# Performance work log

Measured on AMD Instinct MI355X. Metric: run time of the kernel, lower is better.

## Reference

```python
import jax, jax.numpy as jnp
import numpy as np

B = 4
N_TOTAL = 40000
N_SRC0, N_DST0, E0 = 30000, 15000, 360000
N_DST1, E1 = 7500, 180000
D_IN, OUT = 64, 32
H1, C1 = 8, 8
H2, C2 = 1, OUT
NEG_SLOPE = 0.2


def setup_inputs() -> dict:
    key = jax.random.key(0)
    ks = jax.random.split(key, 16)
    inp = {
        'x': jax.random.normal(ks[0], (B, N_TOTAL, D_IN), dtype=jnp.float32),
        'n_id0': jax.random.randint(ks[1], (N_SRC0,), 0, N_SRC0),
        'res_n_id0': jax.random.randint(ks[2], (N_DST0,), 0, N_SRC0),
        'edge_src0': jax.random.randint(ks[3], (E0,), 0, N_SRC0),
        'edge_dst0': jax.random.randint(ks[4], (E0,), 0, N_DST0),
        'res_n_id1': jax.random.randint(ks[5], (N_DST1,), 0, N_DST0),
        'edge_src1': jax.random.randint(ks[6], (E1,), 0, N_DST0),
        'edge_dst1': jax.random.randint(ks[7], (E1,), 0, N_DST1),
        # GATConv params (Glorot-ish scale)
        'W1': jax.random.normal(ks[8], (D_IN, H1 * C1), dtype=jnp.float32) / np.sqrt(D_IN),
        'att_src1': jax.random.normal(ks[9], (H1, C1), dtype=jnp.float32) / np.sqrt(C1),
        'att_dst1': jax.random.normal(ks[10], (H1, C1), dtype=jnp.float32) / np.sqrt(C1),
        'b1': jnp.zeros((H1 * C1,), dtype=jnp.float32),
        'W2': jax.random.normal(ks[11], (H1 * C1, H2 * C2), dtype=jnp.float32) / np.sqrt(H1 * C1),
        'att_src2': jax.random.normal(ks[12], (H2, C2), dtype=jnp.float32) / np.sqrt(C2),
        'att_dst2': jax.random.normal(ks[13], (H2, C2), dtype=jnp.float32) / np.sqrt(C2),
        'b2': jnp.zeros((H2 * C2,), dtype=jnp.float32),
    }
    return inp


def gat_conv(x_src, x_dst, src, dst, W, a_src, a_dst, bias, n_dst, H, C):
    """Bipartite PyG-style GATConv (concat=True, eval mode, no self-loops)."""
    b = x_src.shape[0]
    hs = (x_src @ W).reshape(b, -1, H, C)            # [B, Ns, H, C]
    hd = (x_dst @ W).reshape(b, -1, H, C)            # [B, Nd, H, C]
    es = jnp.einsum('bnhc,hc->bnh', hs, a_src)       # [B, Ns, H]
    ed = jnp.einsum('bnhc,hc->bnh', hd, a_dst)       # [B, Nd, H]
    e = jax.nn.leaky_relu(es[:, src] + ed[:, dst], NEG_SLOPE)  # [B, E, H]
    eT = jnp.swapaxes(e, 0, 1)                       # [E, B, H] (segment over axis 0)
    m = jax.ops.segment_max(eT, dst, num_segments=n_dst)
    p = jnp.exp(eT - m[dst])
    den = jax.ops.segment_sum(p, dst, num_segments=n_dst)
    alpha = p / den[dst]                             # [E, B, H]
    msg = alpha[..., None] * jnp.swapaxes(hs[:, src], 0, 1)    # [E, B, H, C]
    out = jax.ops.segment_sum(msg, dst, num_segments=n_dst)    # [Nd, B, H, C]
    out = jnp.swapaxes(out, 0, 1).reshape(b, n_dst, H * C)
    return out + bias


def reference(x, n_id0, res_n_id0, edge_src0, edge_dst0, res_n_id1, edge_src1,
              edge_dst1, W1, att_src1, att_dst1, b1, W2, att_src2, att_dst2, b2):
    xt = x[:, n_id0, :]                                        # [B, N_SRC0, D_IN]
    h = gat_conv(xt, xt[:, res_n_id0, :], edge_src0, edge_dst0,
                 W1, att_src1, att_dst1, b1, N_DST0, H1, C1)
    h = jax.nn.elu(h)                                          # dropout = identity (eval)
    out = gat_conv(h, h[:, res_n_id1, :], edge_src1, edge_dst1,
                   W2, att_src2, att_dst2, b2, N_DST1, H2, C2)
    return out                                                 # [B, N_DST1, OUT]
```

## Files before the change

### kernel.cpp

```cpp
#include <hip/hip_runtime.h>

#define NB 4
#define NT 40000
#define NS0 30000
#define ND0 15000
#define NE0 360000
#define ND1 7500
#define NE1 180000
#define NEG 0.2f

#define CAP 64
#define K1B ((NB*NS0)/64)
#define SB  ((NE0 + NE1 + 255)/256)

typedef __attribute__((ext_vector_type(8))) short bf8;
typedef __attribute__((ext_vector_type(4))) float f4;

__device__ __forceinline__ unsigned short f2bf(float f) {
    unsigned u = __float_as_uint(f);
    u += 0x7FFF + ((u >> 16) & 1);
    return (unsigned short)(u >> 16);
}
__device__ __forceinline__ float bf_lo(unsigned u) { return __uint_as_float(u << 16); }
__device__ __forceinline__ float bf_hi(unsigned u) { return __uint_as_float(u & 0xFFFF0000u); }

__global__ __launch_bounds__(256) void kA_gemm_scat(
        const float* __restrict__ x, const int* __restrict__ n_id0,
        const float* __restrict__ W1, const float* __restrict__ a_src,
        const float* __restrict__ a_dst,
        unsigned short* __restrict__ ht1b, float* __restrict__ es1, float* __restrict__ ed1,
        const int* __restrict__ esrc0, const int* __restrict__ edst0,
        const int* __restrict__ esrc1, const int* __restrict__ edst1,
        int* __restrict__ cur0, int* __restrict__ cur1,
        int* __restrict__ srcsort0, int* __restrict__ srcsort1) {
    __shared__ unsigned short xtb[64*72];
    __shared__ unsigned short wtb[64*72];
    __shared__ float asl[64], adl[64];
    if (blockIdx.x >= K1B) {
        int t = (blockIdx.x - K1B) * 256 + threadIdx.x;
        if (t < NE0) {
            int d = edst0[t];
            int pos = atomicAdd(&cur0[d], 1);
            if (pos < CAP) srcsort0[d*CAP + pos] = esrc0[t];
        } else if (t < NE0 + NE1) {
            int e = t - NE0;
            int d = edst1[e];
            int pos = atomicAdd(&cur1[d], 1);
            if (pos < CAP) srcsort1[d*CAP + pos] = esrc1[e];
        }
        return;
    }
    int t = threadIdx.x;
    {
        int k = t >> 2, nb = (t & 3) * 16;
        const float* wrow = &W1[k*64 + nb];
        #pragma unroll
        for (int j = 0; j < 16; j += 4) {
            float4 v = *(const float4*)&wrow[j];
            wtb[(nb+j+0)*72 + k] = f2bf(v.x);
            wtb[(nb+j+1)*72 + k] = f2bf(v.y);
            wtb[(nb+j+2)*72 + k] = f2bf(v.z);
            wtb[(nb+j+3)*72 + k] = f2bf(v.w);
        }
    }
    if (t < 64) { asl[t] = a_src[t]; adl[t] = a_dst[t]; }
    {
        int rr = t & 63;
        int q4 = t >> 6;
        int row_s = blockIdx.x * 64 + rr;
        int bs = row_s / NS0;
        int ns = row_s - bs * NS0;
        const float* xrow = x + ((size_t)(bs * NT + n_id0[ns])) * 64;
        #pragma unroll
        for (int j = 0; j < 4; ++j) {
            int k = q4 * 16 + j * 4;
            float4 v = *(const float4*)&xrow[k];
            ushort4 u;
            u.x = f2bf(v.x); u.y = f2bf(v.y); u.z = f2bf(v.z); u.w = f2bf(v.w);
            *(ushort4*)&xtb[rr*72 + k] = u;
        }
    }
    __syncthreads();
    int w = t >> 6, lane = t & 63, quad = lane >> 4, cl = lane & 15;
    int arow = 16*w + cl;
    bf8 a0 = *(const bf8*)&xtb[arow*72 + quad*8];
    bf8 a1 = *(const bf8*)&xtb[arow*72 + 32 + quad*8];
    f4 acc[4];
    #pragma unroll
    for (int sub = 0; sub < 4; ++sub) {
        int n = sub*16 + cl;
        bf8 b0 = *(const bf8*)&wtb[n*72 + quad*8];
        bf8 b1 = *(const bf8*)&wtb[n*72 + 32 + quad*8];
        f4 c = {0.f, 0.f, 0.f, 0.f};
        c = __builtin_amdgcn_mfma_f32_16x16x32_bf16(a0, b0, c, 0, 0, 0);
        c = __builtin_amdgcn_mfma_f32_16x16x32_bf16(a1, b1, c, 0, 0, 0);
        acc[sub] = c;
    }
    int rbase = blockIdx.x*64 + 16*w + quad*4;
    #pragma unroll
    for (int sub = 0; sub < 4; ++sub)
        #pragma unroll
        for (int r = 0; r < 4; ++r)
            ht1b[(size_t)(rbase + r)*64 + sub*16 + cl] = f2bf(acc[sub][r]);
    #pragma unroll
    for (int r = 0; r < 4; ++r) {
        #pragma unroll
        for (int sub = 0; sub < 4; ++sub) {
            int col = sub*16 + cl;
            float ps = acc[sub][r] * asl[col];
            float pd = acc[sub][r] * adl[col];
            ps += __shfl_xor(ps, 1); ps += __shfl_xor(ps, 2); ps += __shfl_xor(ps, 4);
            pd += __shfl_xor(pd, 1); pd += __shfl_xor(pd, 2); pd += __shfl_xor(pd, 4);
            if ((cl & 7) == 0) {
                int h = sub*2 + (cl >> 3);
                es1[(rbase + r)*8 + h] = ps;
                ed1[(rbase + r)*8 + h] = pd;
            }
        }
    }
}

__global__ __launch_bounds__(256) void k3_agg1(
        const int* __restrict__ srcsort0, const int* __restrict__ cur0,
        const int* __restrict__ res0,
        const float* __restrict__ es1, const float* __restrict__ ed1,
        const unsigned short* __restrict__ ht1b, const float* __restrict__ b1,
        float* __restrict__ agg1) {
    int b = blockIdx.x / (ND0/4);
    int chunk = blockIdx.x - b * (ND0/4);
    int d = chunk * 4 + (threadIdx.x >> 6);
    int lane = threadIdx.x & 63;
    int grp = lane >> 3;
    int c = lane & 7;
    int dn = res0[d];
    float edv = ed1[(b*NS0 + dn)*8 + c];
    int start = d * CAP;
    int cnt = cur0[d];
    const float* esb = es1 + (size_t)b*NS0*8;
    const unsigned short* htb = ht1b + (size_t)b*NS0*64;
    float acc[8] = {};
    float wsum = 0.f;
    int i = grp;
    bool v0 = i      < cnt, v1 = i + 8  < cnt,
         v2 = i + 16 < cnt, v3 = i + 24 < cnt;
    int s0 = v0 ? srcsort0[start + i]      : 0;
    int s1 = v1 ? srcsort0[start + i + 8]  : 0;
    int s2 = v2 ? srcsort0[start + i + 16] : 0;
    int s3 = v3 ? srcsort0[start + i + 24] : 0;
    for (;;) {
        float e0 = esb[s0*8 + c], e1 = esb[s1*8 + c];
        float e2 = esb[s2*8 + c], e3 = esb[s3*8 + c];
        uint4 h0 = *(const uint4*)&htb[(size_t)s0*64 + c*8];
        uint4 h1 = *(const uint4*)&htb[(size_t)s1*64 + c*8];
        uint4 h2 = *(const uint4*)&htb[(size_t)s2*64 + c*8];
        uint4 h3 = *(const uint4*)&htb[(size_t)s3*64 + c*8];
        int ni = i + 32;
        bool nv0 = ni      < cnt, nv1 = ni + 8  < cnt,
             nv2 = ni + 16 < cnt, nv3 = ni + 24 < cnt;
        int t0 = nv0 ? srcsort0[start + ni]      : 0;
        int t1 = nv1 ? srcsort0[start + ni + 8]  : 0;
        int t2 = nv2 ? srcsort0[start + ni + 16] : 0;
        int t3 = nv3 ? srcsort0[start + ni + 24] : 0;
        e0 += edv; e1 += edv; e2 += edv; e3 += edv;
        e0 = e0 > 0.f ? e0 : NEG * e0;
        e1 = e1 > 0.f ? e1 : NEG * e1;
        e2 = e2 > 0.f ? e2 : NEG * e2;
        e3 = e3 > 0.f ? e3 : NEG * e3;
        float w0 = v0 ? __expf(e0) : 0.f;
        float w1 = v1 ? __expf(e1) : 0.f;
        float w2 = v2 ? __expf(e2) : 0.f;
        float w3 = v3 ? __expf(e3) : 0.f;
        acc[0] = fmaf(w0, bf_lo(h0.x), acc[0]); acc[1] = fmaf(w0, bf_hi(h0.x), acc[1]);
        acc[2] = fmaf(w0, bf_lo(h0.y), acc[2]); acc[3] = fmaf(w0, bf_hi(h0.y), acc[3]);
        acc[4] = fmaf(w0, bf_lo(h0.z), acc[4]); acc[5] = fmaf(w0, bf_hi(h0.z), acc[5]);
        acc[6] = fmaf(w0, bf_lo(h0.w), acc[6]); acc[7] = fmaf(w0, bf_hi(h0.w), acc[7]);
        acc[0] = fmaf(w1, bf_lo(h1.x), acc[0]); acc[1] = fmaf(w1, bf_hi(h1.x), acc[1]);
        acc[2] = fmaf(w1, bf_lo(h1.y), acc[2]); acc[3] = fmaf(w1, bf_hi(h1.y), acc[3]);
        acc[4] = fmaf(w1, bf_lo(h1.z), acc[4]); acc[5] = fmaf(w1, bf_hi(h1.z), acc[5]);
        acc[6] = fmaf(w1, bf_lo(h1.w), acc[6]); acc[7] = fmaf(w1, bf_hi(h1.w), acc[7]);
        acc[0] = fmaf(w2, bf_lo(h2.x), acc[0]); acc[1] = fmaf(w2, bf_hi(h2.x), acc[1]);
        acc[2] = fmaf(w2, bf_lo(h2.y), acc[2]); acc[3] = fmaf(w2, bf_hi(h2.y), acc[3]);
        acc[4] = fmaf(w2, bf_lo(h2.z), acc[4]); acc[5] = fmaf(w2, bf_hi(h2.z), acc[5]);
        acc[6] = fmaf(w2, bf_lo(h2.w), acc[6]); acc[7] = fmaf(w2, bf_hi(h2.w), acc[7]);
        acc[0] = fmaf(w3, bf_lo(h3.x), acc[0]); acc[1] = fmaf(w3, bf_hi(h3.x), acc[1]);
        acc[2] = fmaf(w3, bf_lo(h3.y), acc[2]); acc[3] = fmaf(w3, bf_hi(h3.y), acc[3]);
        acc[4] = fmaf(w3, bf_lo(h3.z), acc[4]); acc[5] = fmaf(w3, bf_hi(h3.z), acc[5]);
        acc[6] = fmaf(w3, bf_lo(h3.w), acc[6]); acc[7] = fmaf(w3, bf_hi(h3.w), acc[7]);
        wsum += (w0 + w1) + (w2 + w3);
        i = ni; s0 = t0; s1 = t1; s2 = t2; s3 = t3;
        v0 = nv0; v1 = nv1; v2 = nv2; v3 = nv3;
        if (i >= cnt) break;
    }
    #pragma unroll
    for (int j = 0; j < 8; ++j) {
        acc[j] += __shfl_xor(acc[j], 8);
        acc[j] += __shfl_xor(acc[j], 16);
        acc[j] += __shfl_xor(acc[j], 32);
    }
    wsum += __shfl_xor(wsum, 8); wsum += __shfl_xor(wsum, 16); wsum += __shfl_xor(wsum, 32);
    if (grp == 0) {
        float inv = cnt > 0 ? 1.f / wsum : 0.f;
        float4 b_lo = *(const float4*)&b1[c*8];
        float4 b_hi = *(const float4*)&b1[c*8 + 4];
        float o[8];
        o[0] = acc[0]*inv + b_lo.x; o[1] = acc[1]*inv + b_lo.y;
        o[2] = acc[2]*inv + b_lo.z; o[3] = acc[3]*inv + b_lo.w;
        o[4] = acc[4]*inv + b_hi.x; o[5] = acc[5]*inv + b_hi.y;
        o[6] = acc[6]*inv + b_hi.z; o[7] = acc[7]*inv + b_hi.w;
        #pragma unroll
        for (int j = 0; j < 8; ++j) o[j] = o[j] > 0.f ? o[j] : __expf(o[j]) - 1.f;
        float* orow = &agg1[((size_t)(b*ND0 + d))*64 + c*8];
        *(float4*)&orow[0] = make_float4(o[0], o[1], o[2], o[3]);
        *(float4*)&orow[4] = make_float4(o[4], o[5], o[6], o[7]);
    }
}

__global__ __launch_bounds__(256) void k5_node2(
        const float* __restrict__ h, const float* __restrict__ W2,
        const float* __restrict__ a_src2, const float* __restrict__ a_dst2,
        float* __restrict__ ht2, float* __restrict__ es2, float* __restrict__ ed2) {
    __shared__ float xt[64*132];
    __shared__ float Wl[64*32];
    __shared__ float as2[32], ad2[32];
    int t = threadIdx.x;
    for (int i = t; i < 512; i += 256)
        *(float4*)&Wl[i*4] = *(const float4*)&W2[i*4];
    if (t < 32) { as2[t] = a_src2[t]; ad2[t] = a_dst2[t]; }
    int rr = t & 127;
    int q  = t >> 7;
    int row_s = blockIdx.x * 128 + rr;
    bool valid = row_s < NB*ND0;
    const float* hrow = h + (size_t)row_s * 64;
    #pragma unroll
    for (int j = 0; j < 8; ++j) {
        int k = q * 32 + j * 4;
        float4 v = valid ? *(const float4*)&hrow[k] : make_float4(0.f,0.f,0.f,0.f);
        xt[(k+0)*132 + rr] = v.x;
        xt[(k+1)*132 + rr] = v.y;
        xt[(k+2)*132 + rr] = v.z;
        xt[(k+3)*132 + rr] = v.w;
    }
    __syncthreads();
    int c0 = (t & 7) * 4;
    int r0 = (t >> 3) * 4;
    float acc[4][4] = {};
    #pragma unroll 16
    for (int k = 0; k < 64; ++k) {
        float4 a = *(const float4*)&xt[k*132 + r0];
        float4 w = *(const float4*)&Wl[k*32 + c0];
        acc[0][0] = fmaf(a.x, w.x, acc[0][0]); acc[0][1] = fmaf(a.x, w.y, acc[0][1]);
        acc[0][2] = fmaf(a.x, w.z, acc[0][2]); acc[0][3] = fmaf(a.x, w.w, acc[0][3]);
        acc[1][0] = fmaf(a.y, w.x, acc[1][0]); acc[1][1] = fmaf(a.y, w.y, acc[1][1]);
        acc[1][2] = fmaf(a.y, w.z, acc[1][2]); acc[1][3] = fmaf(a.y, w.w, acc[1][3]);
        acc[2][0] = fmaf(a.z, w.x, acc[2][0]); acc[2][1] = fmaf(a.z, w.y, acc[2][1]);
        acc[2][2] = fmaf(a.z, w.z, acc[2][2]); acc[2][3] = fmaf(a.z, w.w, acc[2][3]);
        acc[3][0] = fmaf(a.w, w.x, acc[3][0]); acc[3][1] = fmaf(a.w, w.y, acc[3][1]);
        acc[3][2] = fmaf(a.w, w.z, acc[3][2]); acc[3][3] = fmaf(a.w, w.w, acc[3][3]);
    }
    float s0 = as2[c0], s1 = as2[c0+1], s2 = as2[c0+2], s3 = as2[c0+3];
    float d0 = ad2[c0], d1 = ad2[c0+1], d2 = ad2[c0+2], d3 = ad2[c0+3];
    #pragma unroll
    for (int i = 0; i < 4; ++i) {
        int row = blockIdx.x * 128 + r0 + i;
        float ps = acc[i][0]*s0 + acc[i][1]*s1 + acc[i][2]*s2 + acc[i][3]*s3;
        float pd = acc[i][0]*d0 + acc[i][1]*d1 + acc[i][2]*d2 + acc[i][3]*d3;
        ps += __shfl_xor(ps, 1); ps += __shfl_xor(ps, 2); ps += __shfl_xor(ps, 4);
        pd += __shfl_xor(pd, 1); pd += __shfl_xor(pd, 2); pd += __shfl_xor(pd, 4);
        if (row < NB*ND0) {
            *(float4*)&ht2[(size_t)row*32 + c0] =
                make_float4(acc[i][0], acc[i][1], acc[i][2], acc[i][3]);
            if ((t & 7) == 0) { es2[row] = ps; ed2[row] = pd; }
        }
    }
}

__global__ __launch_bounds__(256) void k7_agg2(
        const int* __restrict__ srcsort1, const int* __restrict__ cur1,
        const int* __restrict__ res1,
        const float* __restrict__ es2, const float* __restrict__ ed2,
        const float* __restrict__ ht2, const float* __restrict__ b2,
        float* __restrict__ outp) {
    int b = blockIdx.x / (ND1/4);
    int chunk = blockIdx.x - b * (ND1/4);
    int d = chunk * 4 + (threadIdx.x >> 6);
    int lane = threadIdx.x & 63;
    int grp = lane >> 3;
    int c = lane & 7;
    int dn = res1[d];
    float edv = ed2[b*ND0 + dn];
    int start = d * CAP;
    int cnt = cur1[d];
    const float* esb = es2 + (size_t)b*ND0;
    const float* htb = ht2 + (size_t)b*ND0*32;
    float ax = 0.f, ay = 0.f, az = 0.f, aw = 0.f, wsum = 0.f;
    int i = grp;
    bool v0 = i      < cnt, v1 = i + 8  < cnt,
         v2 = i + 16 < cnt, v3 = i + 24 < cnt;
    int s0 = v0 ? srcsort1[start + i]      : 0;
    int s1 = v1 ? srcsort1[start + i + 8]  : 0;
    int s2 = v2 ? srcsort1[start + i + 16] : 0;
    int s3 = v3 ? srcsort1[start + i + 24] : 0;
    for (;;) {
        float lg0 = esb[s0], lg1 = esb[s1], lg2 = esb[s2], lg3 = esb[s3];
        float4 h0 = *(const float4*)&htb[(size_t)s0*32 + c*4];
        float4 h1 = *(const float4*)&htb[(size_t)s1*32 + c*4];
        float4 h2 = *(const float4*)&htb[(size_t)s2*32 + c*4];
        float4 h3 = *(const float4*)&htb[(size_t)s3*32 + c*4];
        int ni = i + 32;
        bool nv0 = ni      < cnt, nv1 = ni + 8  < cnt,
             nv2 = ni + 16 < cnt, nv3 = ni + 24 < cnt;
        int t0 = nv0 ? srcsort1[start + ni]      : 0;
        int t1 = nv1 ? srcsort1[start + ni + 8]  : 0;
        int t2 = nv2 ? srcsort1[start + ni + 16] : 0;
        int t3 = nv3 ? srcsort1[start + ni + 24] : 0;
        lg0 += edv; lg1 += edv; lg2 += edv; lg3 += edv;
        lg0 = lg0 > 0.f ? lg0 : NEG * lg0;
        lg1 = lg1 > 0.f ? lg1 : NEG * lg1;
        lg2 = lg2 > 0.f ? lg2 : NEG * lg2;
        lg3 = lg3 > 0.f ? lg3 : NEG * lg3;
        float w0 = v0 ? __expf(lg0) : 0.f;
        float w1 = v1 ? __expf(lg1) : 0.f;
        float w2 = v2 ? __expf(lg2) : 0.f;
        float w3 = v3 ? __expf(lg3) : 0.f;
        ax = fmaf(w0, h0.x, ax); ay = fmaf(w0, h0.y, ay);
        az = fmaf(w0, h0.z, az); aw = fmaf(w0, h0.w, aw);
        ax = fmaf(w1, h1.x, ax); ay = fmaf(w1, h1.y, ay);
        az = fmaf(w1, h1.z, az); aw = fmaf(w1, h1.w, aw);
        ax = fmaf(w2, h2.x, ax); ay = fmaf(w2, h2.y, ay);
        az = fmaf(w2, h2.z, az); aw = fmaf(w2, h2.w, aw);
        ax = fmaf(w3, h3.x, ax); ay = fmaf(w3, h3.y, ay);
        az = fmaf(w3, h3.z, az); aw = fmaf(w3, h3.w, aw);
        wsum += (w0 + w1) + (w2 + w3);
        i = ni; s0 = t0; s1 = t1; s2 = t2; s3 = t3;
        v0 = nv0; v1 = nv1; v2 = nv2; v3 = nv3;
        if (i >= cnt) break;
    }
    ax += __shfl_xor(ax, 8); ax += __shfl_xor(ax, 16); ax += __shfl_xor(ax, 32);
    ay += __shfl_xor(ay, 8); ay += __shfl_xor(ay, 16); ay += __shfl_xor(ay, 32);
    az += __shfl_xor(az, 8); az += __shfl_xor(az, 16); az += __shfl_xor(az, 32);
    aw += __shfl_xor(aw, 8); aw += __shfl_xor(aw, 16); aw += __shfl_xor(aw, 32);
    wsum += __shfl_xor(wsum, 8); wsum += __shfl_xor(wsum, 16); wsum += __shfl_xor(wsum, 32);
    if (grp == 0) {
        float inv = cnt > 0 ? 1.f / wsum : 0.f;
        float4 bb = *(const float4*)&b2[c*4];
        float4 o;
        o.x = ax*inv + bb.x; o.y = ay*inv + bb.y;
        o.z = az*inv + bb.z; o.w = aw*inv + bb.w;
        *(float4*)&outp[((size_t)(b*ND1 + d))*32 + c*4] = o;
    }
}

extern "C" void kernel_launch(void* const* d_in, const int* in_sizes, int n_in,
                              void* d_out, int out_size, void* d_ws, size_t ws_size,
                              hipStream_t stream) {
    const float* x        = (const float*)d_in[0];
    const int*   n_id0    = (const int*)d_in[1];
    const int*   res0     = (const int*)d_in[2];
    const int*   esrc0    = (const int*)d_in[3];
    const int*   edst0    = (const int*)d_in[4];
    const int*   res1     = (const int*)d_in[5];
    const int*   esrc1    = (const int*)d_in[6];
    const int*   edst1    = (const int*)d_in[7];
    const float* W1       = (const float*)d_in[8];
    const float* a_src1   = (const float*)d_in[9];
    const float* a_dst1   = (const float*)d_in[10];
    const float* b1       = (const float*)d_in[11];
    const float* W2       = (const float*)d_in[12];
    const float* a_src2   = (const float*)d_in[13];
    const float* a_dst2   = (const float*)d_in[14];
    const float* b2       = (const float*)d_in[15];
    float* outp = (float*)d_out;

    char* base = (char*)d_ws;
    unsigned short* ht1b = (unsigned short*)base;
    float* es1  = (float*)(base + 15360000);
    float* ed1  = es1 + 960000;
    float* agg1 = ed1 + 960000;
    float* ht2  = agg1 + 3840000;
    float* es2  = ht2 + 1920000;
    float* ed2  = es2 + 60000;
    int* cur0     = (int*)(ed2 + 60000);
    int* cur1     = cur0 + ND0;
    int* srcsort0 = cur1 + ND1;
    int* srcsort1 = srcsort0 + ND0*CAP;

    hipMemsetAsync(cur0, 0, (ND0 + ND1) * sizeof(int), stream);
    kA_gemm_scat<<<K1B + SB, 256, 0, stream>>>(x, n_id0, W1, a_src1, a_dst1,
                                               ht1b, es1, ed1,
                                               esrc0, edst0, esrc1, edst1,
                                               cur0, cur1, srcsort0, srcsort1);
    k3_agg1<<<NB*(ND0/4), 256, 0, stream>>>(srcsort0, cur0, res0, es1, ed1, ht1b, b1, agg1);
    k5_node2<<<(NB*ND0 + 127)/128, 256, 0, stream>>>(agg1, W2, a_src2, a_dst2, ht2, es2, ed2);
    k7_agg2<<<NB*(ND1/4), 256, 0, stream>>>(srcsort1, cur1, res1, es2, ed2, ht2, b2, outp);
}
```

Measured before the change: 209.7 us.

## Fuse layer-2 node transform into layer-1 aggregation and reorder scatter blocks first

The second-layer linear transform and attention projections are folded into the layer-1 aggregation kernel. Each wave keeps its aggregated ELU row in shared memory and multiplies it by W2 there, so the agg1 intermediate no longer goes through global memory and one kernel launch disappears. Separately, the edge-scatter blocks now come before the GEMM blocks in the first kernel. The cost is that every aggregation block loads W2 into LDS and adds a __syncthreads, and its per-row matvec is less efficient than the old tiled GEMM.

```diff
diff --git a/kernel.cpp b/kernel.cpp
--- a/kernel.cpp
+++ b/kernel.cpp
@@ -36,8 +36,8 @@
     __shared__ unsigned short xtb[64*72];
     __shared__ unsigned short wtb[64*72];
     __shared__ float asl[64], adl[64];
-    if (blockIdx.x >= K1B) {
-        int t = (blockIdx.x - K1B) * 256 + threadIdx.x;
+    if (blockIdx.x < SB) {
+        int t = blockIdx.x * 256 + threadIdx.x;
         if (t < NE0) {
             int d = edst0[t];
             int pos = atomicAdd(&cur0[d], 1);
@@ -50,6 +50,7 @@
         }
         return;
     }
+    int bid = blockIdx.x - SB;
     int t = threadIdx.x;
     {
         int k = t >> 2, nb = (t & 3) * 16;
@@ -67,7 +68,7 @@
     {
         int rr = t & 63;
         int q4 = t >> 6;
-        int row_s = blockIdx.x * 64 + rr;
+        int row_s = bid * 64 + rr;
         int bs = row_s / NS0;
         int ns = row_s - bs * NS0;
         const float* xrow = x + ((size_t)(bs * NT + n_id0[ns])) * 64;
@@ -96,7 +97,7 @@
         c = __builtin_amdgcn_mfma_f32_16x16x32_bf16(a1, b1, c, 0, 0, 0);
         acc[sub] = c;
     }
-    int rbase = blockIdx.x*64 + 16*w + quad*4;
+    int rbase = bid*64 + 16*w + quad*4;
     #pragma unroll
     for (int sub = 0; sub < 4; ++sub)
         #pragma unroll
@@ -120,16 +121,26 @@
     }
 }
 
-__global__ __launch_bounds__(256) void k3_agg1(
+__global__ __launch_bounds__(256) void k3_agg1_node2(
         const int* __restrict__ srcsort0, const int* __restrict__ cur0,
         const int* __restrict__ res0,
         const float* __restrict__ es1, const float* __restrict__ ed1,
         const unsigned short* __restrict__ ht1b, const float* __restrict__ b1,
-        float* __restrict__ agg1) {
+        const float* __restrict__ W2, const float* __restrict__ a_src2,
+        const float* __restrict__ a_dst2,
+        float* __restrict__ ht2, float* __restrict__ es2, float* __restrict__ ed2) {
+    __shared__ float W2l[64*32];
+    __shared__ float as2[32], ad2[32];
+    __shared__ float hsh[4][64];
+    int t = threadIdx.x;
+    for (int i = t; i < 512; i += 256)
+        *(float4*)&W2l[i*4] = *(const float4*)&W2[i*4];
+    if (t < 32) { as2[t] = a_src2[t]; ad2[t] = a_dst2[t]; }
     int b = blockIdx.x / (ND0/4);
     int chunk = blockIdx.x - b * (ND0/4);
-    int d = chunk * 4 + (threadIdx.x >> 6);
-    int lane = threadIdx.x & 63;
+    int wv = t >> 6;
+    int d = chunk * 4 + wv;
+    int lane = t & 63;
     int grp = lane >> 3;
     int c = lane & 7;
     int dn = res0[d];
@@ -209,69 +220,26 @@
         o[6] = acc[6]*inv + b_hi.z; o[7] = acc[7]*inv + b_hi.w;
         #pragma unroll
         for (int j = 0; j < 8; ++j) o[j] = o[j] > 0.f ? o[j] : __expf(o[j]) - 1.f;
-        float* orow = &agg1[((size_t)(b*ND0 + d))*64 + c*8];
-        *(float4*)&orow[0] = make_float4(o[0], o[1], o[2], o[3]);
-        *(float4*)&orow[4] = make_float4(o[4], o[5], o[6], o[7]);
-    }
-}
-
-__global__ __launch_bounds__(256) void k5_node2(
-        const float* __restrict__ h, const float* __restrict__ W2,
-        const float* __restrict__ a_src2, const float* __restrict__ a_dst2,
-        float* __restrict__ ht2, float* __restrict__ es2, float* __restrict__ ed2) {
-    __shared__ float xt[64*132];
-    __shared__ float Wl[64*32];
-    __shared__ float as2[32], ad2[32];
-    int t = threadIdx.x;
-    for (int i = t; i < 512; i += 256)
-        *(float4*)&Wl[i*4] = *(const float4*)&W2[i*4];
-    if (t < 32) { as2[t] = a_src2[t]; ad2[t] = a_dst2[t]; }
-    int rr = t & 127;
-    int q  = t >> 7;
-    int row_s = blockIdx.x * 128 + rr;
-    bool valid = row_s < NB*ND0;
-    const float* hrow = h + (size_t)row_s * 64;
-    #pragma unroll
-    for (int j = 0; j < 8; ++j) {
-        int k = q * 32 + j * 4;
-        float4 v = valid ? *(const float4*)&hrow[k] : make_float4(0.f,0.f,0.f,0.f);
-        xt[(k+0)*132 + rr] = v.x;
-        xt[(k+1)*132 + rr] = v.y;
-        xt[(k+2)*132 + rr] = v.z;
-        xt[(k+3)*132 + rr] = v.w;
+        float* hrow = &hsh[wv][c*8];
+        *(float4*)&hrow[0] = make_float4(o[0], o[1], o[2], o[3]);
+        *(float4*)&hrow[4] = make_float4(o[4], o[5], o[6], o[7]);
     }
     __syncthreads();
-    int c0 = (t & 7) * 4;
-    int r0 = (t >> 3) * 4;
-    float acc[4][4] = {};
-    #pragma unroll 16
-    for (int k = 0; k < 64; ++k) {
-        float4 a = *(const float4*)&xt[k*132 + r0];
-        float4 w = *(const float4*)&Wl[k*32 + c0];
-        acc[0][0] = fmaf(a.x, w.x, acc[0][0]); acc[0][1] = fmaf(a.x, w.y, acc[0][1]);
-        acc[0][2] = fmaf(a.x, w.z, acc[0][2]); acc[0][3] = fmaf(a.x, w.w, acc[0][3]);
-        acc[1][0] = fmaf(a.y, w.x, acc[1][0]); acc[1][1] = fmaf(a.y, w.y, acc[1][1]);
-        acc[1][2] = fmaf(a.y, w.z, acc[1][2]); acc[1][3] = fmaf(a.y, w.w, acc[1][3]);
-        acc[2][0] = fmaf(a.z, w.x, acc[2][0]); acc[2][1] = fmaf(a.z, w.y, acc[2][1]);
-        acc[2][2] = fmaf(a.z, w.z, acc[2][2]); acc[2][3] = fmaf(a.z, w.w, acc[2][3]);
-        acc[3][0] = fmaf(a.w, w.x, acc[3][0]); acc[3][1] = fmaf(a.w, w.y, acc[3][1]);
-        acc[3][2] = fmaf(a.w, w.z, acc[3][2]); acc[3][3] = fmaf(a.w, w.w, acc[3][3]);
-    }
-    float s0 = as2[c0], s1 = as2[c0+1], s2 = as2[c0+2], s3 = as2[c0+3];
-    float d0 = ad2[c0], d1 = ad2[c0+1], d2 = ad2[c0+2], d3 = ad2[c0+3];
-    #pragma unroll
-    for (int i = 0; i < 4; ++i) {
-        int row = blockIdx.x * 128 + r0 + i;
-        float ps = acc[i][0]*s0 + acc[i][1]*s1 + acc[i][2]*s2 + acc[i][3]*s3;
-        float pd = acc[i][0]*d0 + acc[i][1]*d1 + acc[i][2]*d2 + acc[i][3]*d3;
-        ps += __shfl_xor(ps, 1); ps += __shfl_xor(ps, 2); ps += __shfl_xor(ps, 4);
-        pd += __shfl_xor(pd, 1); pd += __shfl_xor(pd, 2); pd += __shfl_xor(pd, 4);
-        if (row < NB*ND0) {
-            *(float4*)&ht2[(size_t)row*32 + c0] =
-                make_float4(acc[i][0], acc[i][1], acc[i][2], acc[i][3]);
-            if ((t & 7) == 0) { es2[row] = ps; ed2[row] = pd; }
-        }
-    }
+    int c2 = lane & 31, half = lane >> 5;
+    float acc2 = 0.f;
+    #pragma unroll
+    for (int k = 0; k < 32; ++k)
+        acc2 = fmaf(hsh[wv][half*32 + k], W2l[(half*32 + k)*32 + c2], acc2);
+    acc2 += __shfl_xor(acc2, 32);
+    float ps = acc2 * as2[c2];
+    float pd = acc2 * ad2[c2];
+    ps += __shfl_xor(ps, 1); ps += __shfl_xor(ps, 2); ps += __shfl_xor(ps, 4);
+    ps += __shfl_xor(ps, 8); ps += __shfl_xor(ps, 16);
+    pd += __shfl_xor(pd, 1); pd += __shfl_xor(pd, 2); pd += __shfl_xor(pd, 4);
+    pd += __shfl_xor(pd, 8); pd += __shfl_xor(pd, 16);
+    int row = b*ND0 + d;
+    if (half == 0) ht2[(size_t)row*32 + c2] = acc2;
+    if (lane == 0) { es2[row] = ps; ed2[row] = pd; }
 }
 
 __global__ __launch_bounds__(256) void k7_agg2(
@@ -375,8 +343,7 @@
     unsigned short* ht1b = (unsigned short*)base;
     float* es1  = (float*)(base + 15360000);
     float* ed1  = es1 + 960000;
-    float* agg1 = ed1 + 960000;
-    float* ht2  = agg1 + 3840000;
+    float* ht2  = ed1 + 960000;
     float* es2  = ht2 + 1920000;
     float* ed2  = es2 + 60000;
     int* cur0     = (int*)(ed2 + 60000);
@@ -389,7 +356,7 @@
                                                ht1b, es1, ed1,
                                                esrc0, edst0, esrc1, edst1,
                                                cur0, cur1, srcsort0, srcsort1);
-    k3_agg1<<<NB*(ND0/4), 256, 0, stream>>>(srcsort0, cur0, res0, es1, ed1, ht1b, b1, agg1);
-    k5_node2<<<(NB*ND0 + 127)/128, 256, 0, stream>>>(agg1, W2, a_src2, a_dst2, ht2, es2, ed2);
+    k3_agg1_node2<<<NB*(ND0/4), 256, 0, stream>>>(srcsort0, cur0, res0, es1, ed1, ht1b, b1,
+                                                  W2, a_src2, a_dst2, ht2, es2, ed2);
     k7_agg2<<<NB*(ND1/4), 256, 0, stream>>>(srcsort1, cur1, res1, es2, ed2, ht2, b2, outp);
 }
```

Measured after the change: 207.3 us. Within noise of the previous version (-1.2%).
